# Performance work log

Hardware: AMD Instinct MI355X
Metric: run time of the kernel (lower is better)

Reference implementation:

```python
import jax, jax.numpy as jnp
import numpy as np
from jax import lax

B, S, D = 1, 512, 2048
HK, HV, DK, DV, K = 8, 16, 128, 128, 4
R = HV // HK
KEY_DIM = HK * DK
VAL_DIM = HV * DV
CONV_DIM = 2 * KEY_DIM + VAL_DIM
EPS = 1e-6


def setup_inputs() -> dict:
    key = jax.random.key(0)
    ks = jax.random.split(key, 8)
    hidden_states = jax.random.normal(ks[0], (B, S, D), jnp.float32)
    W_qkvz = jax.random.normal(ks[1], (D, 2 * KEY_DIM + 2 * VAL_DIM), jnp.float32) * 0.02
    W_ba = jax.random.normal(ks[2], (D, 2 * HV), jnp.float32) * 0.02
    conv_w = jax.random.normal(ks[3], (CONV_DIM, 1, K), jnp.float32) * 0.2  # depthwise [C,1,K]
    dt_bias = jnp.ones((HV,), jnp.float32)
    A_log = jnp.log(jax.random.uniform(ks[4], (HV,), jnp.float32, 1e-3, 16.0))
    norm_weight = jnp.ones((DV,), jnp.float32)
    W_out = jax.random.normal(ks[5], (VAL_DIM, D), jnp.float32) * 0.02
    return dict(hidden_states=hidden_states, W_qkvz=W_qkvz, W_ba=W_ba, conv_w=conv_w,
                dt_bias=dt_bias, A_log=A_log, norm_weight=norm_weight, W_out=W_out)


def _l2norm(x):
    return x * lax.rsqrt(jnp.sum(x * x, -1, keepdims=True) + EPS)


def reference(hidden_states, W_qkvz, W_ba, conv_w, dt_bias, A_log, norm_weight, W_out):
    # input projections
    qkvz = hidden_states @ W_qkvz              # [B,S,2*key_dim+2*value_dim]
    ba = hidden_states @ W_ba                  # [B,S,2*HV]
    # _rearrange: split per key-head group
    qkvz = qkvz.reshape(B, S, HK, 2 * DK + 2 * R * DV)
    q = qkvz[..., :DK]                                         # [B,S,HK,DK]
    k = qkvz[..., DK:2 * DK]                                   # [B,S,HK,DK]
    v = qkvz[..., 2 * DK:2 * DK + R * DV].reshape(B, S, HV, DV)
    z = qkvz[..., 2 * DK + R * DV:].reshape(B, S, HV, DV)
    ba = ba.reshape(B, S, HK, 2 * R)
    b = ba[..., :R].reshape(B, S, HV)
    a = ba[..., R:].reshape(B, S, HV)
    # fused causal depthwise conv1d + SiLU over concat(q,k,v)
    mixed = jnp.concatenate([q.reshape(B, S, -1), k.reshape(B, S, -1), v.reshape(B, S, -1)], -1)
    mixed = mixed.transpose(0, 2, 1)           # [B,C,S]
    mixed = lax.conv_general_dilated(mixed, conv_w, (1,), [(K - 1, 0)],
                                     feature_group_count=CONV_DIM,
                                     dimension_numbers=('NCH', 'OIH', 'NCH'))
    mixed = jax.nn.silu(mixed).transpose(0, 2, 1)  # [B,S,C]
    q = mixed[..., :KEY_DIM].reshape(B, S, HK, DK)
    k = mixed[..., KEY_DIM:2 * KEY_DIM].reshape(B, S, HK, DK)
    v = mixed[..., 2 * KEY_DIM:].reshape(B, S, HV, DV)
    # gates
    beta = jax.nn.sigmoid(b)                                   # [B,S,HV]
    g = jnp.exp(-jnp.exp(A_log) * jax.nn.softplus(a + dt_bias))  # per-step decay in (0,1)
    q = _l2norm(q) * (DK ** -0.5)
    k = _l2norm(k)
    q = jnp.repeat(q, R, axis=2)               # GQA expand to HV heads
    k = jnp.repeat(k, R, axis=2)
    # gated delta-rule recurrence over sequence (state per batch/head: [DK,DV])
    def step(Sst, inp):
        qt, kt, vt, gt, bt = inp
        Sst = Sst * gt[..., None, None]
        pred = jnp.einsum('bhk,bhkv->bhv', kt, Sst)
        delta = (vt - pred) * bt[..., None]
        Sst = Sst + jnp.einsum('bhk,bhv->bhkv', kt, delta)
        o = jnp.einsum('bhk,bhkv->bhv', qt, Sst)
        return Sst, o
    xs = (q.transpose(1, 0, 2, 3), k.transpose(1, 0, 2, 3), v.transpose(1, 0, 2, 3),
          g.transpose(1, 0, 2), beta.transpose(1, 0, 2))
    S0 = jnp.zeros((B, HV, DK, DV), jnp.float32)
    _, core = lax.scan(step, S0, xs)           # core: [S,B,HV,DV]
    core = core.transpose(1, 0, 2, 3)          # [B,S,HV,DV]
    # gated RMSNorm per value head, gated by silu(z)
    var = jnp.mean(core * core, -1, keepdims=True)
    normed = core * lax.rsqrt(var + EPS) * norm_weight * jax.nn.silu(z)
    return normed.reshape(B, S, VAL_DIM) @ W_out
```

## Files before the change

kernel.cpp:

```cpp
#include <hip/hip_runtime.h>
#include <hip/hip_bf16.h>
#include <math.h>

#define S_  512
#define D_  2048
#define HK_ 8
#define HV_ 16
#define DK_ 128
#define DV_ 128
#define KEY_DIM_ 1024
#define VAL_DIM_ 2048
#define QKVZ_N  6144
#define EPS_ 1e-6f
#define SPAD_ (S_ + 8)

typedef __attribute__((ext_vector_type(8))) short short8;
typedef __attribute__((ext_vector_type(4))) float f32x4;
typedef __attribute__((ext_vector_type(2))) float v2f;
typedef unsigned short ushort_t;
typedef unsigned int uint_t;

__device__ __forceinline__ ushort_t f2bf(float x) {
    uint_t u = __float_as_uint(x);
    return (ushort_t)((u + 0x7FFFu + ((u >> 16) & 1u)) >> 16);
}

__device__ __forceinline__ void gl2lds16(const void* g, void* l) {
    __builtin_amdgcn_global_load_lds((const __attribute__((address_space(1))) uint_t*)g,
                                     (__attribute__((address_space(3))) uint_t*)l, 16, 0, 0);
}
__device__ __forceinline__ void gl2lds4(const void* g, void* l) {
    __builtin_amdgcn_global_load_lds((const __attribute__((address_space(1))) uint_t*)g,
                                     (__attribute__((address_space(3))) uint_t*)l, 4, 0, 0);
}

__global__ __launch_bounds__(256) void convert_bf16(const float* __restrict__ X,
                                                    ushort_t* __restrict__ H, int n4) {
    int i = blockIdx.x * blockDim.x + threadIdx.x;
    if (i >= n4) return;
    float4 v = ((const float4*)X)[i];
    ushort4 h;
    h.x = f2bf(v.x); h.y = f2bf(v.y); h.z = f2bf(v.z); h.w = f2bf(v.w);
    ((ushort4*)H)[i] = h;
}

__global__ __launch_bounds__(256) void transpose_convert(const float* __restrict__ W,
                                                         ushort_t* __restrict__ Th,
                                                         int K, int N) {
    __shared__ float tile[64][65];
    const int kb = blockIdx.y * 64, nb = blockIdx.x * 64;
    const int t = threadIdx.x;
#pragma unroll
    for (int i = 0; i < 4; ++i) {
        int r = (t >> 4) + i * 16;
        int c4 = (t & 15) * 4;
        float4 v = *(const float4*)&W[(size_t)(kb + r) * N + nb + c4];
        tile[r][c4 + 0] = v.x; tile[r][c4 + 1] = v.y;
        tile[r][c4 + 2] = v.z; tile[r][c4 + 3] = v.w;
    }
    __syncthreads();
#pragma unroll
    for (int i = 0; i < 4; ++i) {
        int idx = t + 256 * i;
        int n = idx >> 4;
        int k4 = (idx & 15) * 4;
        ushort4 h;
        h.x = f2bf(tile[k4 + 0][n]); h.y = f2bf(tile[k4 + 1][n]);
        h.z = f2bf(tile[k4 + 2][n]); h.w = f2bf(tile[k4 + 3][n]);
        *(ushort4*)&Th[(size_t)(nb + n) * K + kb + k4] = h;
    }
}

template<int BM, int BN, int WR, int WC>
__global__ __launch_bounds__(256) void gemm_bf16(const ushort_t* __restrict__ A,
                                                 const ushort_t* __restrict__ B,
                                                 float* __restrict__ C,
                                                 int M, int N, int K) {
    constexpr int TM = BM / (16 * WR);
    constexpr int TN = BN / (16 * WC);
    constexpr int AI = (BM / 16) * 2;
    constexpr int BI = (BN / 16) * 2;

    __shared__ __align__(16) ushort_t sA[2][2][BM][32];
    __shared__ __align__(16) ushort_t sB[2][2][BN][32];

    const int t = threadIdx.x;
    const int w = t >> 6, lane = t & 63;
    const int wr = w / WC, wc = w % WC;
    const int lm = lane & 15, quad = lane >> 4;
    const int m0 = blockIdx.y * BM, n0 = blockIdx.x * BN;
    const int lrow = lane >> 2;
    const int lch  = (lane & 3) * 8;

    auto stage = [&](int buf, int k0) {
#pragma unroll
        for (int j = w; j < AI; j += 4) {
            int ks = j & 1, r0 = (j >> 1) * 16;
            gl2lds16(&A[(size_t)(m0 + r0 + lrow) * K + k0 + ks * 32 + lch],
                     &sA[buf][ks][r0][0]);
        }
#pragma unroll
        for (int j = w; j < BI; j += 4) {
            int ks = j & 1, r0 = (j >> 1) * 16;
            gl2lds16(&B[(size_t)(n0 + r0 + lrow) * K + k0 + ks * 32 + lch],
                     &sB[buf][ks][r0][0]);
        }
    };

    f32x4 acc[TM][TN] = {};
    stage(0, 0);
    __syncthreads();

    const int NK = K / 64;
    for (int it = 0; it < NK; ++it) {
        int buf = it & 1;
        if (it + 1 < NK) stage(buf ^ 1, (it + 1) * 64);
#pragma unroll
        for (int ks = 0; ks < 2; ++ks) {
            short8 bf[TN];
#pragma unroll
            for (int ni = 0; ni < TN; ++ni)
                bf[ni] = *(const short8*)&sB[buf][ks][wc * (TN * 16) + ni * 16 + lm][quad * 8];
#pragma unroll
            for (int mi = 0; mi < TM; ++mi) {
                short8 af = *(const short8*)&sA[buf][ks][wr * (TM * 16) + mi * 16 + lm][quad * 8];
#pragma unroll
                for (int ni = 0; ni < TN; ++ni)
                    acc[mi][ni] = __builtin_amdgcn_mfma_f32_16x16x32_bf16(af, bf[ni], acc[mi][ni], 0, 0, 0);
            }
        }
        __syncthreads();
    }

#pragma unroll
    for (int mi = 0; mi < TM; ++mi)
#pragma unroll
        for (int ni = 0; ni < TN; ++ni) {
            int row = m0 + wr * TM * 16 + mi * 16 + quad * 4;
            int col = n0 + wc * TN * 16 + ni * 16 + lm;
#pragma unroll
            for (int r = 0; r < 4; ++r)
                C[(size_t)(row + r) * N + col] = acc[mi][ni][r];
        }
}

__global__ __launch_bounds__(256) void ba_kernel(const float* __restrict__ hid,
                                                 const float* __restrict__ Wba,
                                                 float* __restrict__ ba) {
    const int s = blockIdx.x;
    const int j = threadIdx.x & 31;
    const int kg = threadIdx.x >> 5;
    const float* h = hid + (size_t)s * D_;
    float sum = 0.f;
    const int k0 = kg * 256;
#pragma unroll 8
    for (int k = k0; k < k0 + 256; ++k)
        sum = fmaf(h[k], Wba[(size_t)k * 32 + j], sum);
    __shared__ float red[8][32];
    red[kg][j] = sum;
    __syncthreads();
    if (threadIdx.x < 32) {
        float tot = 0.f;
#pragma unroll
        for (int r = 0; r < 8; ++r) tot += red[r][j];
        ba[s * 32 + j] = tot;
    }
}

__global__ __launch_bounds__(128) void conv_kernel(const float* __restrict__ qkvz,
                                                   const float* __restrict__ conv_w,
                                                   float* __restrict__ qc,
                                                   float* __restrict__ kc,
                                                   float* __restrict__ vc) {
    const int s   = blockIdx.x;
    const int grp = blockIdx.y;
    const int d   = threadIdx.x;

    int col, c;
    if (grp < 8) {
        int hk = grp;
        col = hk * 768 + d;
        c   = hk * 128 + d;
    } else if (grp < 16) {
        int hk = grp - 8;
        col = hk * 768 + 128 + d;
        c   = 1024 + (hk * 128 + d);
    } else {
        int hv = grp - 16;
        col = (hv >> 1) * 768 + 256 + (hv & 1) * 128 + d;
        c   = 2048 + (hv * 128 + d);
    }

    const float w0 = conv_w[c * 4 + 0];
    const float w1 = conv_w[c * 4 + 1];
    const float w2 = conv_w[c * 4 + 2];
    const float w3 = conv_w[c * 4 + 3];

    float x = 0.f;
    if (s - 3 >= 0) x += qkvz[(size_t)(s - 3) * QKVZ_N + col] * w0;
    if (s - 2 >= 0) x += qkvz[(size_t)(s - 2) * QKVZ_N + col] * w1;
    if (s - 1 >= 0) x += qkvz[(size_t)(s - 1) * QKVZ_N + col] * w2;
    x += qkvz[(size_t)s * QKVZ_N + col] * w3;

    x = x / (1.f + expf(-x));

    if (grp < 16) {
        float ss = x * x;
#pragma unroll
        for (int m = 1; m < 64; m <<= 1) ss += __shfl_xor(ss, m);
        __shared__ float red[2];
        int wid = threadIdx.x >> 6;
        if ((threadIdx.x & 63) == 0) red[wid] = ss;
        __syncthreads();
        float tot = red[0] + red[1];
        float scale = rsqrtf(tot + EPS_);
        if (grp < 8) {
            x = x * scale * 0.08838834764831845f;
            qc[((size_t)s * HK_ + grp) * DK_ + d] = x;
        } else {
            x = x * scale;
            kc[((size_t)s * HK_ + (grp - 8)) * DK_ + d] = x;
        }
    } else {
        vc[((size_t)s * HV_ + (grp - 16)) * DV_ + d] = x;
    }
}

template<int CTRL>
__device__ __forceinline__ float dpp_xor(float x) {
    int v = __builtin_amdgcn_update_dpp(0, __float_as_int(x), CTRL, 0xF, 0xF, true);
    return __int_as_float(v);
}
__device__ __forceinline__ float red16(float x) {
    x += dpp_xor<0xB1>(x);
    x += dpp_xor<0x4E>(x);
    x += dpp_xor<0x141>(x);
    x += dpp_xor<0x140>(x);
    return x;
}
__device__ __forceinline__ float red32(float x) {
    x = red16(x);
    x += __int_as_float(__builtin_amdgcn_ds_swizzle(__float_as_int(x), 0x401F));
    return x;
}

__device__ __forceinline__ float gate_g(float a, float Aexp) {
    float sp = (a > 20.f) ? a : log1pf(expf(a));
    return expf(-Aexp * sp);
}

__global__ __launch_bounds__(256) void scal_kernel(const float* __restrict__ kc,
                                                   const float* __restrict__ qc,
                                                   const float* __restrict__ ba,
                                                   const float* __restrict__ A_log,
                                                   const float* __restrict__ dt_bias,
                                                   float* __restrict__ scal) {
    const int t  = blockIdx.x;
    const int hk = threadIdx.x >> 5;
    const int l  = threadIdx.x & 31;

    const float* kt = &kc[((size_t)t * HK_ + hk) * DK_ + l * 4];
    const float* qt = &qc[((size_t)t * HK_ + hk) * DK_ + l * 4];
    const float4 zz = {0.f, 0.f, 0.f, 0.f};
    float4 k0 = *(const float4*)kt;
    float4 q0 = *(const float4*)qt;
    float4 k1 = (t >= 1) ? *(const float4*)(kt - (size_t)HK_ * DK_)     : zz;
    float4 k2 = (t >= 2) ? *(const float4*)(kt - (size_t)2 * HK_ * DK_) : zz;
    float4 k3 = (t >= 3) ? *(const float4*)(kt - (size_t)3 * HK_ * DK_) : zz;

    auto dot4 = [](float4 a, float4 b) { return a.x*b.x + a.y*b.y + a.z*b.z + a.w*b.w; };
    float c1 = red32(dot4(k0, k1));
    float c2 = red32(dot4(k0, k2));
    float c3 = red32(dot4(k0, k3));
    float d0 = red32(dot4(q0, k0));
    float d1 = red32(dot4(q0, k1));
    float d2 = red32(dot4(q0, k2));
    float d3 = red32(dot4(q0, k3));

    if (l < 2) {
        int h = hk * 2 + l;
        float Aexp = expf(A_log[h]);
        float dtb  = dt_bias[h];
        float bv = ba[t * 32 + hk * 4 + l];
        float av = ba[t * 32 + hk * 4 + 2 + l];
        float be = 1.f / (1.f + expf(-bv));
        float g0 = gate_g(av + dtb, Aexp);
        float g1 = 1.f, g2 = 1.f, g3 = 1.f;
        if (t >= 1) g1 = gate_g(ba[(t - 1) * 32 + hk * 4 + 2 + l] + dtb, Aexp);
        if (t >= 2) g2 = gate_g(ba[(t - 2) * 32 + hk * 4 + 2 + l] + dtb, Aexp);
        if (t >= 3) g3 = gate_g(ba[(t - 3) * 32 + hk * 4 + 2 + l] + dtb, Aexp);
        float G2 = g0 * g1, G3 = G2 * g2, G4 = G3 * g3;
        float4 oC = {g0, be, G4, 0.f};
        float4 oA = {-be * g0 * c1, -be * G2 * c2, -be * G3 * c3, -be * G4};
        float4 oB = {d0, g0 * d1, G2 * d2, G3 * d3};
        float* dst = &scal[(size_t)(h * SPAD_ + t) * 16];
        *(float4*)&dst[0]  = oC;
        *(float4*)&dst[4]  = oA;
        *(float4*)&dst[8]  = oB;
        *(float4*)&dst[12] = zz;
    }
}

__global__ __launch_bounds__(128) void scan_kernel(const float* __restrict__ qc,
                                                   const float* __restrict__ kc,
                                                   const float* __restrict__ vc,
                                                   const float* __restrict__ scal,
                                                   float* __restrict__ core) {
    const int h = blockIdx.y, v0 = blockIdx.x * 8;
    const int tid = threadIdx.x;
    const int w = tid >> 6, lane = tid & 63;
    const int sub = lane & 15, colg = lane >> 4;
    const int vloc = w * 4 + colg;
    const int v = v0 + vloc;
    const int hk = h >> 1;

    __shared__ __align__(16) float skq[2][32][256];
    __shared__ __align__(16) float sv[2][32][8];
    __shared__ __align__(16) float ssc[2][32][16];
    __shared__ __align__(16) float hkq[2][4][256];
    __shared__ __align__(16) float hv[2][4][8];
    __shared__ __align__(16) float hsc[2][4][16];

    auto stage_chunk = [&](int buf, int c) {
        const int t0 = c * 32;
        for (int j = w * 16; j < w * 16 + 16; ++j) {
            int tt = t0 + j;
            const float* src = (lane < 32)
                ? &kc[((size_t)tt * HK_ + hk) * DK_ + lane * 4]
                : &qc[((size_t)tt * HK_ + hk) * DK_ + (lane - 32) * 4];
            gl2lds16(src, &skq[buf][j][0]);
        }
        if (w == 0) {
#pragma unroll
            for (int i = 0; i < 4; ++i) {
                int tt = t0 + i * 8 + (lane >> 3);
                gl2lds4(&vc[((size_t)tt * HV_ + h) * DV_ + v0 + (lane & 7)],
                        &sv[buf][i * 8][0]);
            }
        } else {
#pragma unroll
            for (int i = 0; i < 2; ++i)
                gl2lds16(&scal[(size_t)(h * SPAD_ + t0) * 16 + i * 256 + lane * 4],
                         &ssc[buf][i * 16][0]);
        }
    };
    auto stage_head = [&](int c) {
        const int hb = c & 1;
        const int t0 = c * 32;
        if (w == 1) {
#pragma unroll
            for (int j = 0; j < 4; ++j) {
                int tt = t0 + j;
                const float* src = (lane < 32)
                    ? &kc[((size_t)tt * HK_ + hk) * DK_ + lane * 4]
                    : &qc[((size_t)tt * HK_ + hk) * DK_ + (lane - 32) * 4];
                gl2lds16(src, &hkq[hb][j][0]);
            }
        } else {
            if (lane < 32)
                gl2lds4(&vc[((size_t)(t0 + (lane >> 3)) * HV_ + h) * DV_ + v0 + (lane & 7)],
                        &hv[hb][0][0]);
            if (lane < 16)
                gl2lds16(&scal[(size_t)(h * SPAD_ + t0) * 16 + lane * 4],
                         &hsc[hb][0][0]);
        }
    };

    v2f Sr[4] = {};
    v2f kR[8][4] = {};
    v2f qR[4][4] = {};
    float vR[4] = {};
    float4 scA[4] = {}, scB[4] = {}, scC[4] = {};
    float U[4] = {}, V[4] = {}, dl[4] = {};

    stage_chunk(0, 0);
    stage_head(1);
    __syncthreads();

#pragma unroll
    for (int p = 0; p < 4; ++p)
#pragma unroll
        for (int i = 0; i < 4; ++i) {
            kR[p][i] = *(const v2f*)&skq[0][p][sub * 8 + i * 2];
            qR[p][i] = *(const v2f*)&skq[0][p][128 + sub * 8 + i * 2];
        }
#pragma unroll
    for (int p = 0; p < 2; ++p) {
        scC[p] = *(const float4*)&ssc[0][p][0];
        scA[p] = *(const float4*)&ssc[0][p][4];
        scB[p] = *(const float4*)&ssc[0][p][8];
        vR[p] = sv[0][p][vloc];
    }

    for (int c = 0; c < 16; ++c) {
        const int buf = c & 1;
        const int hb = (c + 1) & 1;
        if (c + 1 < 16) stage_chunk(buf ^ 1, c + 1);
        if (c + 2 < 16) stage_head(c + 2);
        const int t0 = c * 32;

#pragma unroll
        for (int j = 0; j < 32; ++j) {
            {
                const float g  = ((const float*)&scC[(j + 2) & 3])[0];
                const float dd = dl[(j + 2) & 3];
                const v2f g2 = {g, g}, dd2 = {dd, dd};
#pragma unroll
                for (int i = 0; i < 4; ++i)
                    Sr[i] = kR[(j + 6) & 7][i] * dd2 + g2 * Sr[i];
            }
            {
                const float* kb = (j < 28) ? &skq[buf][j + 4][0] : &hkq[hb][j - 28][0];
#pragma unroll
                for (int i = 0; i < 4; ++i) {
                    kR[(j + 4) & 7][i] = *(const v2f*)&kb[sub * 8 + i * 2];
                    qR[(j + 4) & 3][i] = *(const v2f*)&kb[128 + sub * 8 + i * 2];
                }
            }
            {
                const float* sb = (j < 30) ? &ssc[buf][j + 2][0] : &hsc[hb][j - 30][0];
                scC[(j + 2) & 3] = *(const float4*)&sb[0];
                scA[(j + 2) & 3] = *(const float4*)&sb[4];
                scB[(j + 2) & 3] = *(const float4*)&sb[8];
                const float* vb = (j < 30) ? &sv[buf][j + 2][0] : &hv[hb][j - 30][0];
                vR[(j + 2) & 3] = vb[vloc];
            }
            {
                v2f ua = kR[(j + 2) & 7][0] * Sr[0] + kR[(j + 2) & 7][1] * Sr[1]
                       + kR[(j + 2) & 7][2] * Sr[2] + kR[(j + 2) & 7][3] * Sr[3];
                v2f va = qR[(j + 2) & 3][0] * Sr[0] + qR[(j + 2) & 3][1] * Sr[1]
                       + qR[(j + 2) & 3][2] * Sr[2] + qR[(j + 2) & 3][3] * Sr[3];
                U[(j + 2) & 3] = red16(ua.x + ua.y);
                V[(j + 2) & 3] = red16(va.x + va.y);
            }
            {
                const float4 A = scA[j & 3], B = scB[j & 3], Cc = scC[j & 3];
                const float d1 = dl[(j + 3) & 3], d2 = dl[(j + 2) & 3], d3 = dl[(j + 1) & 3];
                const float E = fmaf(A.w, U[j & 3], Cc.y * vR[j & 3]);
                const float X = fmaf(A.y, d2, fmaf(A.z, d3, E));
                const float dn = fmaf(A.x, d1, X);
                const float o = fmaf(B.x, dn, fmaf(B.y, d1,
                                  fmaf(B.z, d2, fmaf(B.w, d3, Cc.z * V[j & 3]))));
                if (sub == 0)
                    core[((size_t)(t0 + j) * HV_ + h) * DV_ + v] = o;
                dl[j & 3] = dn;
            }
        }
        __syncthreads();
    }
}

__global__ __launch_bounds__(128) void normgate_kernel(const float* __restrict__ core,
                                                       const float* __restrict__ qkvz,
                                                       const float* __restrict__ nw,
                                                       ushort_t* __restrict__ nh) {
    const int s  = blockIdx.x;
    const int hv = blockIdx.y;
    const int d  = threadIdx.x;

    float x = core[((size_t)s * HV_ + hv) * DV_ + d];
    float ss = x * x;
#pragma unroll
    for (int m = 1; m < 64; m <<= 1) ss += __shfl_xor(ss, m);
    __shared__ float red[2];
    int wid = threadIdx.x >> 6;
    if ((threadIdx.x & 63) == 0) red[wid] = ss;
    __syncthreads();
    float var = (red[0] + red[1]) * (1.f / 128.f);
    float rs  = rsqrtf(var + EPS_);

    float z  = qkvz[(size_t)s * QKVZ_N + (hv >> 1) * 768 + 512 + (hv & 1) * 128 + d];
    float sz = z / (1.f + expf(-z));

    float y = x * rs * nw[d] * sz;
    nh[(size_t)s * VAL_DIM_ + hv * DV_ + d] = f2bf(y);
}

extern "C" void kernel_launch(void* const* d_in, const int* in_sizes, int n_in,
                              void* d_out, int out_size, void* d_ws, size_t ws_size,
                              hipStream_t stream) {
    const float* hidden  = (const float*)d_in[0];
    const float* W_qkvz  = (const float*)d_in[1];
    const float* W_ba    = (const float*)d_in[2];
    const float* conv_w  = (const float*)d_in[3];
    const float* dt_bias = (const float*)d_in[4];
    const float* A_log   = (const float*)d_in[5];
    const float* norm_w  = (const float*)d_in[6];
    const float* W_out   = (const float*)d_in[7];
    float* out = (float*)d_out;

    char* w = (char*)d_ws;
    auto alloc = [&](size_t bytes) { char* p = w; w += (bytes + 255) & ~(size_t)255; return p; };

    float*    qkvz = (float*)alloc((size_t)S_ * QKVZ_N * 4);
    float*    ba   = (float*)alloc((size_t)S_ * 32 * 4);
    float*    qc   = (float*)alloc((size_t)SPAD_ * KEY_DIM_ * 4);
    float*    kc   = (float*)alloc((size_t)SPAD_ * KEY_DIM_ * 4);
    float*    vc   = (float*)alloc((size_t)SPAD_ * VAL_DIM_ * 4);
    float*    scal = (float*)alloc((size_t)HV_ * SPAD_ * 16 * 4);
    float*    core = (float*)alloc((size_t)S_ * VAL_DIM_ * 4);
    ushort_t* hidh = (ushort_t*)alloc((size_t)S_ * D_ * 2);
    ushort_t* nrmh = (ushort_t*)alloc((size_t)S_ * VAL_DIM_ * 2);
    ushort_t* Wqh  = (ushort_t*)alloc((size_t)D_ * QKVZ_N * 2);
    ushort_t* Woh  = (ushort_t*)alloc((size_t)VAL_DIM_ * D_ * 2);

    convert_bf16<<<dim3((S_ * D_ / 4 + 255) / 256), 256, 0, stream>>>(hidden, hidh, S_ * D_ / 4);
    transpose_convert<<<dim3(QKVZ_N / 64, D_ / 64), 256, 0, stream>>>(W_qkvz, Wqh, D_, QKVZ_N);
    transpose_convert<<<dim3(D_ / 64, VAL_DIM_ / 64), 256, 0, stream>>>(W_out, Woh, VAL_DIM_, D_);

    gemm_bf16<64, 128, 1, 4><<<dim3(QKVZ_N / 128, S_ / 64), 256, 0, stream>>>(
        hidh, Wqh, qkvz, S_, QKVZ_N, D_);

    ba_kernel<<<dim3(S_), 256, 0, stream>>>(hidden, W_ba, ba);

    conv_kernel<<<dim3(S_, 32), 128, 0, stream>>>(qkvz, conv_w, qc, kc, vc);

    scal_kernel<<<dim3(S_), 256, 0, stream>>>(kc, qc, ba, A_log, dt_bias, scal);

    scan_kernel<<<dim3(DV_ / 8, HV_), 128, 0, stream>>>(qc, kc, vc, scal, core);

    normgate_kernel<<<dim3(S_, HV_), 128, 0, stream>>>(core, qkvz, norm_w, nrmh);

    gemm_bf16<64, 64, 2, 2><<<dim3(D_ / 64, S_ / 64), 256, 0, stream>>>(
        nrmh, Woh, out, S_, D_, VAL_DIM_);
}
```

Baseline: 287.1 us.

## Fuse prep kernels into one launch and restructure scan scalar loads via readlane

Merges the hidden-state bf16 conversion, both weight transpose-converts and the ba projection into a single prep_kernel launch, and widens the transpose stores to 16-byte writes. In the scan kernel, per-step scalar coefficients are no longer staged through LDS. Each lane now holds one timestep's scalars in registers, loaded one chunk ahead, and broadcasts them with readlane. The state and k/q register tiles move from float2 to float4 vectors. This cuts launch overhead and LDS traffic in the serial scan, at the cost of more registers and a more complex scalar pipeline.

```diff
diff --git a/kernel.cpp b/kernel.cpp
--- a/kernel.cpp
+++ b/kernel.cpp
@@ -16,7 +16,6 @@
 
 typedef __attribute__((ext_vector_type(8))) short short8;
 typedef __attribute__((ext_vector_type(4))) float f32x4;
-typedef __attribute__((ext_vector_type(2))) float v2f;
 typedef unsigned short ushort_t;
 typedef unsigned int uint_t;
 
@@ -34,22 +33,13 @@
                                      (__attribute__((address_space(3))) uint_t*)l, 4, 0, 0);
 }
 
-__global__ __launch_bounds__(256) void convert_bf16(const float* __restrict__ X,
-                                                    ushort_t* __restrict__ H, int n4) {
-    int i = blockIdx.x * blockDim.x + threadIdx.x;
-    if (i >= n4) return;
-    float4 v = ((const float4*)X)[i];
-    ushort4 h;
-    h.x = f2bf(v.x); h.y = f2bf(v.y); h.z = f2bf(v.z); h.w = f2bf(v.w);
-    ((ushort4*)H)[i] = h;
-}
-
-__global__ __launch_bounds__(256) void transpose_convert(const float* __restrict__ W,
-                                                         ushort_t* __restrict__ Th,
-                                                         int K, int N) {
-    __shared__ float tile[64][65];
-    const int kb = blockIdx.y * 64, nb = blockIdx.x * 64;
-    const int t = threadIdx.x;
+#define RL(x, l) __int_as_float(__builtin_amdgcn_readlane(__float_as_int(x), (l)))
+
+__device__ __forceinline__ void transpose_body(const float* __restrict__ W,
+                                               ushort_t* __restrict__ Th,
+                                               int K, int N, int kb, int nb,
+                                               int t, float* smem) {
+    float (*tile)[65] = (float(*)[65])smem;
 #pragma unroll
     for (int i = 0; i < 4; ++i) {
         int r = (t >> 4) + i * 16;
@@ -60,14 +50,60 @@
     }
     __syncthreads();
 #pragma unroll
-    for (int i = 0; i < 4; ++i) {
+    for (int i = 0; i < 2; ++i) {
         int idx = t + 256 * i;
-        int n = idx >> 4;
-        int k4 = (idx & 15) * 4;
+        int n = idx >> 3;
+        int k8 = (idx & 7) * 8;
+        ushort_t p[8];
+#pragma unroll
+        for (int r = 0; r < 8; ++r) p[r] = f2bf(tile[k8 + r][n]);
+        *(uint4*)&Th[(size_t)(nb + n) * K + kb + k8] = *(const uint4*)p;
+    }
+}
+
+__global__ __launch_bounds__(256) void prep_kernel(const float* __restrict__ hidden,
+                                                   const float* __restrict__ W_qkvz,
+                                                   const float* __restrict__ W_out,
+                                                   const float* __restrict__ Wba,
+                                                   ushort_t* __restrict__ hidh,
+                                                   ushort_t* __restrict__ Wqh,
+                                                   ushort_t* __restrict__ Woh,
+                                                   float* __restrict__ ba) {
+    __shared__ float smem[64 * 65];
+    const int id = blockIdx.x;
+    const int t = threadIdx.x;
+
+    if (id < 1024) {
+        int i = id * 256 + t;
+        float4 v = ((const float4*)hidden)[i];
         ushort4 h;
-        h.x = f2bf(tile[k4 + 0][n]); h.y = f2bf(tile[k4 + 1][n]);
-        h.z = f2bf(tile[k4 + 2][n]); h.w = f2bf(tile[k4 + 3][n]);
-        *(ushort4*)&Th[(size_t)(nb + n) * K + kb + k4] = h;
+        h.x = f2bf(v.x); h.y = f2bf(v.y); h.z = f2bf(v.z); h.w = f2bf(v.w);
+        ((ushort4*)hidh)[i] = h;
+    } else if (id < 1024 + 3072) {
+        int lid = id - 1024;
+        transpose_body(W_qkvz, Wqh, D_, QKVZ_N, (lid / 96) * 64, (lid % 96) * 64, t, smem);
+    } else if (id < 1024 + 3072 + 1024) {
+        int lid = id - 4096;
+        transpose_body(W_out, Woh, D_, D_, (lid / 32) * 64, (lid % 32) * 64, t, smem);
+    } else {
+        const int s = id - 5120;
+        const int j = t & 31;
+        const int kg = t >> 5;
+        const float* h = hidden + (size_t)s * D_;
+        float sum = 0.f;
+        const int k0 = kg * 256;
+#pragma unroll 8
+        for (int k = k0; k < k0 + 256; ++k)
+            sum = fmaf(h[k], Wba[(size_t)k * 32 + j], sum);
+        float (*red)[32] = (float(*)[32])smem;
+        red[kg][j] = sum;
+        __syncthreads();
+        if (t < 32) {
+            float tot = 0.f;
+#pragma unroll
+            for (int r = 0; r < 8; ++r) tot += red[r][j];
+            ba[s * 32 + j] = tot;
+        }
     }
 }
 
@@ -142,29 +178,6 @@
             for (int r = 0; r < 4; ++r)
                 C[(size_t)(row + r) * N + col] = acc[mi][ni][r];
         }
-}
-
-__global__ __launch_bounds__(256) void ba_kernel(const float* __restrict__ hid,
-                                                 const float* __restrict__ Wba,
-                                                 float* __restrict__ ba) {
-    const int s = blockIdx.x;
-    const int j = threadIdx.x & 31;
-    const int kg = threadIdx.x >> 5;
-    const float* h = hid + (size_t)s * D_;
-    float sum = 0.f;
-    const int k0 = kg * 256;
-#pragma unroll 8
-    for (int k = k0; k < k0 + 256; ++k)
-        sum = fmaf(h[k], Wba[(size_t)k * 32 + j], sum);
-    __shared__ float red[8][32];
-    red[kg][j] = sum;
-    __syncthreads();
-    if (threadIdx.x < 32) {
-        float tot = 0.f;
-#pragma unroll
-        for (int r = 0; r < 8; ++r) tot += red[r][j];
-        ba[s * 32 + j] = tot;
-    }
 }
 
 __global__ __launch_bounds__(128) void conv_kernel(const float* __restrict__ qkvz,
@@ -316,10 +329,8 @@
 
     __shared__ __align__(16) float skq[2][32][256];
     __shared__ __align__(16) float sv[2][32][8];
-    __shared__ __align__(16) float ssc[2][32][16];
     __shared__ __align__(16) float hkq[2][4][256];
-    __shared__ __align__(16) float hv[2][4][8];
-    __shared__ __align__(16) float hsc[2][4][16];
+    __shared__ __align__(16) float hvb[2][4][8];
 
     auto stage_chunk = [&](int buf, int c) {
         const int t0 = c * 32;
@@ -337,11 +348,6 @@
                 gl2lds4(&vc[((size_t)tt * HV_ + h) * DV_ + v0 + (lane & 7)],
                         &sv[buf][i * 8][0]);
             }
-        } else {
-#pragma unroll
-            for (int i = 0; i < 2; ++i)
-                gl2lds16(&scal[(size_t)(h * SPAD_ + t0) * 16 + i * 256 + lane * 4],
-                         &ssc[buf][i * 16][0]);
         }
     };
     auto stage_head = [&](int c) {
@@ -359,38 +365,39 @@
         } else {
             if (lane < 32)
                 gl2lds4(&vc[((size_t)(t0 + (lane >> 3)) * HV_ + h) * DV_ + v0 + (lane & 7)],
-                        &hv[hb][0][0]);
-            if (lane < 16)
-                gl2lds16(&scal[(size_t)(h * SPAD_ + t0) * 16 + lane * 4],
-                         &hsc[hb][0][0]);
+                        &hvb[hb][0][0]);
         }
     };
 
-    v2f Sr[4] = {};
-    v2f kR[8][4] = {};
-    v2f qR[4][4] = {};
-    float vR[4] = {};
-    float4 scA[4] = {}, scB[4] = {}, scC[4] = {};
-    float U[4] = {}, V[4] = {}, dl[4] = {};
+    auto ldsc = [&](int c, float4& o0, float4& o1, float4& o2) {
+        const float* p = &scal[(size_t)(h * SPAD_ + c * 32 + (lane & 31)) * 16];
+        o0 = *(const float4*)p;
+        o1 = *(const float4*)(p + 4);
+        o2 = *(const float4*)(p + 8);
+    };
+
+    f32x4 Sr[2] = {};
+    f32x4 kR[8][2] = {}, qR[4][2] = {};
+    float vR[4] = {}, U[4] = {}, V[4] = {}, dl[4] = {};
+    float4 cur0 = {0,0,0,0}, cur1 = {0,0,0,0}, cur2 = {0,0,0,0};
+    float4 nxt0 = {0,0,0,0}, nxt1 = {0,0,0,0}, nxt2 = {0,0,0,0};
+    float4 prv0 = {0,0,0,0};
 
     stage_chunk(0, 0);
     stage_head(1);
+    ldsc(0, cur0, cur1, cur2);
+    ldsc(1, nxt0, nxt1, nxt2);
     __syncthreads();
 
 #pragma unroll
-    for (int p = 0; p < 4; ++p)
-#pragma unroll
-        for (int i = 0; i < 4; ++i) {
-            kR[p][i] = *(const v2f*)&skq[0][p][sub * 8 + i * 2];
-            qR[p][i] = *(const v2f*)&skq[0][p][128 + sub * 8 + i * 2];
-        }
-#pragma unroll
-    for (int p = 0; p < 2; ++p) {
-        scC[p] = *(const float4*)&ssc[0][p][0];
-        scA[p] = *(const float4*)&ssc[0][p][4];
-        scB[p] = *(const float4*)&ssc[0][p][8];
-        vR[p] = sv[0][p][vloc];
-    }
+    for (int p = 0; p < 4; ++p) {
+        kR[p][0] = *(const f32x4*)&skq[0][p][4 * sub];
+        kR[p][1] = *(const f32x4*)&skq[0][p][64 + 4 * sub];
+        qR[p][0] = *(const f32x4*)&skq[0][p][128 + 4 * sub];
+        qR[p][1] = *(const f32x4*)&skq[0][p][192 + 4 * sub];
+    }
+    vR[0] = sv[0][0][vloc];
+    vR[1] = sv[0][1][vloc];
 
     for (int c = 0; c < 16; ++c) {
         const int buf = c & 1;
@@ -402,51 +409,48 @@
 #pragma unroll
         for (int j = 0; j < 32; ++j) {
             {
-                const float g  = ((const float*)&scC[(j + 2) & 3])[0];
+                const float g  = (j >= 2) ? RL(cur0.x, j - 2) : RL(prv0.x, 30 + j);
                 const float dd = dl[(j + 2) & 3];
-                const v2f g2 = {g, g}, dd2 = {dd, dd};
-#pragma unroll
-                for (int i = 0; i < 4; ++i)
-                    Sr[i] = kR[(j + 6) & 7][i] * dd2 + g2 * Sr[i];
+                const f32x4 g4 = {g, g, g, g};
+                const f32x4 dd4 = {dd, dd, dd, dd};
+                Sr[0] = kR[(j + 6) & 7][0] * dd4 + g4 * Sr[0];
+                Sr[1] = kR[(j + 6) & 7][1] * dd4 + g4 * Sr[1];
             }
             {
                 const float* kb = (j < 28) ? &skq[buf][j + 4][0] : &hkq[hb][j - 28][0];
-#pragma unroll
-                for (int i = 0; i < 4; ++i) {
-                    kR[(j + 4) & 7][i] = *(const v2f*)&kb[sub * 8 + i * 2];
-                    qR[(j + 4) & 3][i] = *(const v2f*)&kb[128 + sub * 8 + i * 2];
-                }
-            }
+                kR[(j + 4) & 7][0] = *(const f32x4*)&kb[4 * sub];
+                kR[(j + 4) & 7][1] = *(const f32x4*)&kb[64 + 4 * sub];
+                qR[(j + 4) & 3][0] = *(const f32x4*)&kb[128 + 4 * sub];
+                qR[(j + 4) & 3][1] = *(const f32x4*)&kb[192 + 4 * sub];
+            }
+            vR[(j + 2) & 3] = (j < 30) ? sv[buf][j + 2][vloc] : hvb[hb][j - 30][vloc];
             {
-                const float* sb = (j < 30) ? &ssc[buf][j + 2][0] : &hsc[hb][j - 30][0];
-                scC[(j + 2) & 3] = *(const float4*)&sb[0];
-                scA[(j + 2) & 3] = *(const float4*)&sb[4];
-                scB[(j + 2) & 3] = *(const float4*)&sb[8];
-                const float* vb = (j < 30) ? &sv[buf][j + 2][0] : &hv[hb][j - 30][0];
-                vR[(j + 2) & 3] = vb[vloc];
+                f32x4 ku = kR[(j + 2) & 7][0] * Sr[0] + kR[(j + 2) & 7][1] * Sr[1];
+                f32x4 qu = qR[(j + 2) & 3][0] * Sr[0] + qR[(j + 2) & 3][1] * Sr[1];
+                U[(j + 2) & 3] = red16((ku[0] + ku[1]) + (ku[2] + ku[3]));
+                V[(j + 2) & 3] = red16((qu[0] + qu[1]) + (qu[2] + qu[3]));
             }
             {
-                v2f ua = kR[(j + 2) & 7][0] * Sr[0] + kR[(j + 2) & 7][1] * Sr[1]
-                       + kR[(j + 2) & 7][2] * Sr[2] + kR[(j + 2) & 7][3] * Sr[3];
-                v2f va = qR[(j + 2) & 3][0] * Sr[0] + qR[(j + 2) & 3][1] * Sr[1]
-                       + qR[(j + 2) & 3][2] * Sr[2] + qR[(j + 2) & 3][3] * Sr[3];
-                U[(j + 2) & 3] = red16(ua.x + ua.y);
-                V[(j + 2) & 3] = red16(va.x + va.y);
-            }
-            {
-                const float4 A = scA[j & 3], B = scB[j & 3], Cc = scC[j & 3];
+                const float be = RL(cur0.y, j), G4 = RL(cur0.z, j);
+                const float a1 = RL(cur1.x, j), a2 = RL(cur1.y, j);
+                const float a3 = RL(cur1.z, j), bU = RL(cur1.w, j);
+                const float w0 = RL(cur2.x, j), w1 = RL(cur2.y, j);
+                const float w2 = RL(cur2.z, j), w3 = RL(cur2.w, j);
                 const float d1 = dl[(j + 3) & 3], d2 = dl[(j + 2) & 3], d3 = dl[(j + 1) & 3];
-                const float E = fmaf(A.w, U[j & 3], Cc.y * vR[j & 3]);
-                const float X = fmaf(A.y, d2, fmaf(A.z, d3, E));
-                const float dn = fmaf(A.x, d1, X);
-                const float o = fmaf(B.x, dn, fmaf(B.y, d1,
-                                  fmaf(B.z, d2, fmaf(B.w, d3, Cc.z * V[j & 3]))));
+                const float E = fmaf(bU, U[j & 3], be * vR[j & 3]);
+                const float X = fmaf(a2, d2, fmaf(a3, d3, E));
+                const float dn = fmaf(a1, d1, X);
+                const float o = fmaf(w0, dn, fmaf(w1, d1,
+                                  fmaf(w2, d2, fmaf(w3, d3, G4 * V[j & 3]))));
                 if (sub == 0)
                     core[((size_t)(t0 + j) * HV_ + h) * DV_ + v] = o;
                 dl[j & 3] = dn;
             }
         }
         __syncthreads();
+        prv0 = cur0;
+        cur0 = nxt0; cur1 = nxt1; cur2 = nxt2;
+        if (c + 2 < 16) ldsc(c + 2, nxt0, nxt1, nxt2);
     }
 }
 
@@ -504,15 +508,12 @@
     ushort_t* Wqh  = (ushort_t*)alloc((size_t)D_ * QKVZ_N * 2);
     ushort_t* Woh  = (ushort_t*)alloc((size_t)VAL_DIM_ * D_ * 2);
 
-    convert_bf16<<<dim3((S_ * D_ / 4 + 255) / 256), 256, 0, stream>>>(hidden, hidh, S_ * D_ / 4);
-    transpose_convert<<<dim3(QKVZ_N / 64, D_ / 64), 256, 0, stream>>>(W_qkvz, Wqh, D_, QKVZ_N);
-    transpose_convert<<<dim3(D_ / 64, VAL_DIM_ / 64), 256, 0, stream>>>(W_out, Woh, VAL_DIM_, D_);
+    prep_kernel<<<dim3(5632), 256, 0, stream>>>(hidden, W_qkvz, W_out, W_ba,
+                                                hidh, Wqh, Woh, ba);
 
     gemm_bf16<64, 128, 1, 4><<<dim3(QKVZ_N / 128, S_ / 64), 256, 0, stream>>>(
         hidh, Wqh, qkvz, S_, QKVZ_N, D_);
 
-    ba_kernel<<<dim3(S_), 256, 0, stream>>>(hidden, W_ba, ba);
-
     conv_kernel<<<dim3(S_, 32), 128, 0, stream>>>(qkvz, conv_w, qc, kc, vc);
 
     scal_kernel<<<dim3(S_), 256, 0, stream>>>(kc, qc, ba, A_log, dt_bias, scal);
```

Result: slower. 296.7 us (+3.4%).
